# Kernel optimization log

Measured on AMD Instinct MI355X. Metric: run time of the kernel, lower is better.

The kernel has to match this reference:

```python
import jax, jax.numpy as jnp
import numpy as np

N_NODES = 100000
N_EDGES = 1600000
IN_CH = 128
HID = 128   # 2 * out_channels
OUT_CH = 64


def setup_inputs() -> dict:
    key = jax.random.key(0)
    k1, k2, k3, k4, k5, k6 = jax.random.split(key, 6)
    x = jax.random.normal(k1, (N_NODES, IN_CH), dtype=jnp.float32)
    edge_index = jax.random.randint(k2, (2, N_EDGES), 0, N_NODES, dtype=jnp.int64)
    W1 = jax.random.normal(k3, (IN_CH, HID), dtype=jnp.float32) / np.sqrt(IN_CH)
    b1 = jax.random.normal(k4, (HID,), dtype=jnp.float32) * 0.01
    W2 = jax.random.normal(k5, (HID, OUT_CH), dtype=jnp.float32) / np.sqrt(HID)
    b2 = jax.random.normal(k6, (OUT_CH,), dtype=jnp.float32) * 0.01
    return {"x": x, "edge_index": edge_index, "W1": W1, "b1": b1, "W2": W2, "b2": b2}


def _gcn_layer(x, src, dst, norm, W, b, n_nodes):
    # GCNConv: linear transform, then normalized scatter-add aggregation + bias
    h = x @ W                                   # [N, d_out]
    msg = h[src] * norm[:, None]                # gather + edge normalize, [E+N, d_out]
    out = jax.ops.segment_sum(msg, dst, num_segments=n_nodes)
    return out + b


def reference(x, edge_index, W1, b1, W2, b2):
    n = x.shape[0]
    loop = jnp.arange(n, dtype=edge_index.dtype)
    # add self-loops (PyG GCNConv default)
    src = jnp.concatenate([edge_index[0], loop])
    dst = jnp.concatenate([edge_index[1], loop])
    # symmetric normalization deg^-1/2[src] * deg^-1/2[dst]
    deg = jax.ops.segment_sum(jnp.ones_like(dst, x.dtype), dst, num_segments=n)
    dinv = jnp.where(deg > 0, jax.lax.rsqrt(deg), 0.0)
    norm = dinv[src] * dinv[dst]

    h = jax.nn.relu(_gcn_layer(x, src, dst, norm, W1, b1, n))
    out = jax.nn.relu(_gcn_layer(h, src, dst, norm, W2, b2, n))
    return out
```

## Files before the change

kernel.cpp:

```cpp
#include <hip/hip_runtime.h>
#include <hip/hip_fp16.h>

#define BSH 9
#define BSZ 512
#define CAP 12288

__global__ __launch_bounds__(256) void passA(const int* __restrict__ ei,
                                             int* __restrict__ bcount, int E, int NB) {
  __shared__ int hist[256];
  int t = threadIdx.x;
  hist[t] = 0;
  __syncthreads();
  for (int e = blockIdx.x * 256 + t; e < E; e += gridDim.x * 256)
    atomicAdd(&hist[ei[E + e] >> BSH], 1);
  __syncthreads();
  if (t < NB && hist[t]) atomicAdd(&bcount[t], hist[t]);
}

__global__ __launch_bounds__(256) void scanB(const int* __restrict__ bcount,
                                             int* __restrict__ bstart,
                                             int* __restrict__ bfill, int NB, int E) {
  __shared__ int s[256];
  int t = threadIdx.x;
  int v = (t < NB) ? bcount[t] : 0;
  s[t] = v;
  __syncthreads();
  for (int off = 1; off < 256; off <<= 1) {
    int add = (t >= off) ? s[t - off] : 0;
    __syncthreads();
    s[t] += add;
    __syncthreads();
  }
  if (t < NB) {
    int ex = s[t] - v;
    bstart[t] = ex;
    bfill[t] = ex;
  }
  if (t == 0) bstart[NB] = E;
}

template <int NT, bool IN_F16, bool SCALE>
__device__ __forceinline__ void gemm_body(const void* __restrict__ Xv,
                                          const float* __restrict__ W,
                                          const float* __restrict__ dinv,
                                          __half* __restrict__ G, int nrows, int bid,
                                          float4* Xs, float4* Ws) {
  constexpr int TN4 = NT / 64;
  constexpr int KT = 16;
  constexpr int NW4 = NT / 4;
  const float4* W4 = (const float4*)W;
  int tid = threadIdx.x;
  int tx = tid & 15, ty = (tid >> 4) & 3;
  int tyg = tid >> 4;
  int row0 = bid * 128;

  float acc[8][TN4][4];
#pragma unroll
  for (int r = 0; r < 8; ++r)
#pragma unroll
    for (int c = 0; c < TN4; ++c)
#pragma unroll
      for (int q = 0; q < 4; ++q) acc[r][c][q] = 0.f;

  for (int k0 = 0; k0 < 128; k0 += KT) {
    if constexpr (!IN_F16) {
      const float4* X4 = (const float4*)Xv;
#pragma unroll
      for (int u = 0; u < 2; ++u) {
        int f = tid + u * 256;
        int r = f >> 2, kq = f & 3;
        int gr = row0 + r;
        float4 v = {0.f, 0.f, 0.f, 0.f};
        if (gr < nrows) v = X4[gr * 32 + (k0 >> 2) + kq];
        Xs[r * 4 + kq] = v;
      }
    } else {
      const float4* X4h = (const float4*)Xv;
      int r = tid >> 1, oct = tid & 1;
      int gr = row0 + r;
      float4 raw = {0.f, 0.f, 0.f, 0.f};
      if (gr < nrows) raw = X4h[gr * 16 + (k0 >> 3) + oct];
      const __half2* hp = (const __half2*)&raw;
      float2 f0 = __half22float2(hp[0]);
      float2 f1 = __half22float2(hp[1]);
      float2 f2 = __half22float2(hp[2]);
      float2 f3 = __half22float2(hp[3]);
      Xs[r * 4 + oct * 2 + 0] = make_float4(f0.x, f0.y, f1.x, f1.y);
      Xs[r * 4 + oct * 2 + 1] = make_float4(f2.x, f2.y, f3.x, f3.y);
    }
#pragma unroll
    for (int u = 0; u < (KT * NW4 + 255) / 256; ++u) {
      int f = tid + u * 256;
      if (f < KT * NW4) {
        int k = f / NW4, c = f % NW4;
        Ws[f] = W4[(size_t)(k0 + k) * NW4 + c];
      }
    }
    __syncthreads();
#pragma unroll
    for (int k4 = 0; k4 < KT / 4; ++k4) {
      int kk4 = (k4 + ty) & 3;
      float4 xa[8];
#pragma unroll
      for (int r = 0; r < 8; ++r) xa[r] = Xs[(tyg * 8 + r) * 4 + kk4];
      float4 wv[4][TN4];
#pragma unroll
      for (int kk = 0; kk < 4; ++kk)
#pragma unroll
        for (int c = 0; c < TN4; ++c)
          wv[kk][c] = Ws[(kk4 * 4 + kk) * NW4 + tx * TN4 + c];
#pragma unroll
      for (int r = 0; r < 8; ++r) {
        float xk[4] = {xa[r].x, xa[r].y, xa[r].z, xa[r].w};
#pragma unroll
        for (int kk = 0; kk < 4; ++kk)
#pragma unroll
          for (int c = 0; c < TN4; ++c) {
            acc[r][c][0] = fmaf(xk[kk], wv[kk][c].x, acc[r][c][0]);
            acc[r][c][1] = fmaf(xk[kk], wv[kk][c].y, acc[r][c][1]);
            acc[r][c][2] = fmaf(xk[kk], wv[kk][c].z, acc[r][c][2]);
            acc[r][c][3] = fmaf(xk[kk], wv[kk][c].w, acc[r][c][3]);
          }
      }
    }
    __syncthreads();
  }
  float2* G2 = (float2*)G;
#pragma unroll
  for (int r = 0; r < 8; ++r) {
    int gr = row0 + tyg * 8 + r;
    if (gr < nrows) {
      float d = SCALE ? dinv[gr] : 1.f;
#pragma unroll
      for (int c = 0; c < TN4; ++c) {
        union { __half2 h[2]; float2 f; } u;
        u.h[0] = __floats2half2_rn(acc[r][c][0] * d, acc[r][c][1] * d);
        u.h[1] = __floats2half2_rn(acc[r][c][2] * d, acc[r][c][3] * d);
        G2[(size_t)gr * (NT / 4) + tx * TN4 + c] = u.f;
      }
    }
  }
}

__global__ __launch_bounds__(256) void fused_gemm_passB(
    const float* __restrict__ X, const float* __restrict__ W1,
    __half* __restrict__ G, int nrows, int GB,
    const int* __restrict__ ei, int* __restrict__ bfill,
    unsigned int* __restrict__ pairs, int E) {
  if ((int)blockIdx.x < GB) {
    __shared__ float4 Xs[128 * 4];
    __shared__ float4 Ws[16 * 32];
    gemm_body<128, false, false>(X, W1, nullptr, G, nrows, blockIdx.x, Xs, Ws);
  } else {
    __shared__ int hist[256];
    __shared__ int gbase[256];
    int bid = blockIdx.x - GB;
    int t = threadIdx.x;
    hist[t] = 0;
    __syncthreads();
    int d[8], s[8], lp[8], bb[8];
    int base = bid * 2048;
#pragma unroll
    for (int u = 0; u < 8; ++u) {
      int e = base + u * 256 + t;
      if (e < E) {
        d[u] = ei[E + e];
        s[u] = ei[e];
        bb[u] = d[u] >> BSH;
        lp[u] = atomicAdd(&hist[bb[u]], 1);
      } else {
        bb[u] = -1;
      }
    }
    __syncthreads();
    if (hist[t]) gbase[t] = atomicAdd(&bfill[t], hist[t]);
    __syncthreads();
#pragma unroll
    for (int u = 0; u < 8; ++u)
      if (bb[u] >= 0)
        pairs[gbase[bb[u]] + lp[u]] =
            ((unsigned int)(d[u] & (BSZ - 1)) << 17) | (unsigned int)s[u];
  }
}

__global__ __launch_bounds__(512) void passC(const unsigned int* __restrict__ pairs,
                                             const int* __restrict__ bstart,
                                             int* __restrict__ rowstart,
                                             int* __restrict__ deg,
                                             float* __restrict__ dinv,
                                             int* __restrict__ csr, int N) {
  __shared__ int hcnt[BSZ];
  __shared__ int lfill[BSZ];
  __shared__ int ss[512];
  __shared__ int lcsr[CAP];
  int b = blockIdx.x;
  int t = threadIdx.x;
  int lo = bstart[b], hi = bstart[b + 1];
  int cnt = hi - lo;
  int nbase = b << BSH;
  hcnt[t] = 0;
  __syncthreads();
  for (int k = lo + t; k < hi; k += 512)
    atomicAdd(&hcnt[(pairs[k] >> 17) & (BSZ - 1)], 1);
  __syncthreads();
  int v = hcnt[t];
  ss[t] = v;
  __syncthreads();
  for (int off = 1; off < 512; off <<= 1) {
    int add = (t >= off) ? ss[t - off] : 0;
    __syncthreads();
    ss[t] += add;
    __syncthreads();
  }
  int ex = ss[t] - v;
  lfill[t] = ex;
  int node = nbase + t;
  if (node < N) {
    rowstart[node] = lo + ex;
    deg[node] = v;
    dinv[node] = rsqrtf((float)(v + 1));
  }
  __syncthreads();
  bool fits = (cnt <= CAP);
  for (int k = lo + t; k < hi; k += 512) {
    unsigned int p = pairs[k];
    int pos = atomicAdd(&lfill[(p >> 17) & (BSZ - 1)], 1);
    int src = (int)(p & 0x1FFFFu);
    if (fits) lcsr[pos] = src;
    else      csr[lo + pos] = src;
  }
  __syncthreads();
  if (fits)
    for (int k = t; k < cnt; k += 512) csr[lo + k] = lcsr[k];
}

__global__ __launch_bounds__(256) void agg128(
    const __half* __restrict__ G, const int* __restrict__ csr,
    const int* __restrict__ rowstart, const int* __restrict__ deg,
    const float* __restrict__ dinv, const float* __restrict__ bias,
    __half* __restrict__ out, int n) {
  int wid = blockIdx.x * 4 + (threadIdx.x >> 6);
  if (wid >= n) return;
  int i = __builtin_amdgcn_readfirstlane(wid);
  int lane = threadIdx.x & 63;
  const __half2* Gp = (const __half2*)G;
  float di = dinv[i];
  float2 g = __half22float2(Gp[(size_t)i * 64 + lane]);
  float2 a = {di * g.x, di * g.y};
  int s = rowstart[i];
  int d = deg[i];
  int cnt = d < 64 ? d : 64;
  int myidx = 0;
  if (lane < cnt) myidx = csr[s + lane];
  int k = 0;
  for (; k + 3 < cnt; k += 4) {
    int s0 = __builtin_amdgcn_readfirstlane(__shfl(myidx, k));
    int s1 = __builtin_amdgcn_readfirstlane(__shfl(myidx, k + 1));
    int s2 = __builtin_amdgcn_readfirstlane(__shfl(myidx, k + 2));
    int s3 = __builtin_amdgcn_readfirstlane(__shfl(myidx, k + 3));
    float w0 = dinv[s0], w1 = dinv[s1], w2 = dinv[s2], w3 = dinv[s3];
    float2 v0 = __half22float2(Gp[(size_t)s0 * 64 + lane]);
    float2 v1 = __half22float2(Gp[(size_t)s1 * 64 + lane]);
    float2 v2 = __half22float2(Gp[(size_t)s2 * 64 + lane]);
    float2 v3 = __half22float2(Gp[(size_t)s3 * 64 + lane]);
    a.x = fmaf(w0, v0.x, a.x); a.y = fmaf(w0, v0.y, a.y);
    a.x = fmaf(w1, v1.x, a.x); a.y = fmaf(w1, v1.y, a.y);
    a.x = fmaf(w2, v2.x, a.x); a.y = fmaf(w2, v2.y, a.y);
    a.x = fmaf(w3, v3.x, a.x); a.y = fmaf(w3, v3.y, a.y);
  }
  for (; k < cnt; ++k) {
    int s0 = __builtin_amdgcn_readfirstlane(__shfl(myidx, k));
    float w0 = dinv[s0];
    float2 v0 = __half22float2(Gp[(size_t)s0 * 64 + lane]);
    a.x = fmaf(w0, v0.x, a.x); a.y = fmaf(w0, v0.y, a.y);
  }
  for (int j = s + 64; j < s + d; ++j) {
    int s0 = __builtin_amdgcn_readfirstlane(csr[j]);
    float w0 = dinv[s0];
    float2 v0 = __half22float2(Gp[(size_t)s0 * 64 + lane]);
    a.x = fmaf(w0, v0.x, a.x); a.y = fmaf(w0, v0.y, a.y);
  }
  float2 b = ((const float2*)bias)[lane];
  float ox = fmaxf(fmaf(di, a.x, b.x), 0.f);
  float oy = fmaxf(fmaf(di, a.y, b.y), 0.f);
  ((__half2*)out)[(size_t)i * 64 + lane] = __floats2half2_rn(ox, oy);
}

__global__ __launch_bounds__(256) void agg64(
    const __half* __restrict__ G, const int* __restrict__ csr,
    const int* __restrict__ rowstart, const int* __restrict__ deg,
    const float* __restrict__ dinv, const float* __restrict__ bias,
    float* __restrict__ out, int n) {
  int wid = blockIdx.x * 4 + (threadIdx.x >> 6);
  if (wid >= n) return;
  int i = __builtin_amdgcn_readfirstlane(wid);
  int lane = threadIdx.x & 63;
  float a = __half2float(G[(size_t)i * 64 + lane]);
  int s = rowstart[i];
  int d = deg[i];
  int cnt = d < 64 ? d : 64;
  int myidx = 0;
  if (lane < cnt) myidx = csr[s + lane];
  int k = 0;
  for (; k + 3 < cnt; k += 4) {
    int s0 = __builtin_amdgcn_readfirstlane(__shfl(myidx, k));
    int s1 = __builtin_amdgcn_readfirstlane(__shfl(myidx, k + 1));
    int s2 = __builtin_amdgcn_readfirstlane(__shfl(myidx, k + 2));
    int s3 = __builtin_amdgcn_readfirstlane(__shfl(myidx, k + 3));
    float v0 = __half2float(G[(size_t)s0 * 64 + lane]);
    float v1 = __half2float(G[(size_t)s1 * 64 + lane]);
    float v2 = __half2float(G[(size_t)s2 * 64 + lane]);
    float v3 = __half2float(G[(size_t)s3 * 64 + lane]);
    a += (v0 + v1) + (v2 + v3);
  }
  for (; k < cnt; ++k) {
    int s0 = __builtin_amdgcn_readfirstlane(__shfl(myidx, k));
    a += __half2float(G[(size_t)s0 * 64 + lane]);
  }
  for (int j = s + 64; j < s + d; ++j) {
    int s0 = __builtin_amdgcn_readfirstlane(csr[j]);
    a += __half2float(G[(size_t)s0 * 64 + lane]);
  }
  float o = fmaxf(fmaf(dinv[i], a, bias[lane]), 0.f);
  out[(size_t)i * 64 + lane] = o;
}

__global__ __launch_bounds__(256) void gemm64(const __half* __restrict__ X,
                                              const float* __restrict__ W,
                                              const float* __restrict__ dinv,
                                              __half* __restrict__ G, int nrows) {
  __shared__ float4 Xs[128 * 4];
  __shared__ float4 Ws[16 * 16];
  gemm_body<64, true, true>(X, W, dinv, G, nrows, blockIdx.x, Xs, Ws);
}

extern "C" void kernel_launch(void* const* d_in, const int* in_sizes, int n_in,
                              void* d_out, int out_size, void* d_ws, size_t ws_size,
                              hipStream_t stream) {
  const float* x  = (const float*)d_in[0];
  const int*   ei = (const int*)d_in[1];
  const float* W1 = (const float*)d_in[2];
  const float* b1 = (const float*)d_in[3];
  const float* W2 = (const float*)d_in[4];
  const float* b2 = (const float*)d_in[5];
  float* out = (float*)d_out;

  const int N = in_sizes[0] / 128;
  const int E = in_sizes[1] / 2;
  const int NB = (N + BSZ - 1) >> BSH;

  char* base = (char*)d_ws;
  size_t off = 0;
  auto alloc = [&](size_t bytes) -> void* {
    void* p = base + off;
    off += (bytes + 255) & ~(size_t)255;
    return p;
  };
  int*          bcount   = (int*)alloc(256 * 4);
  int*          bstart   = (int*)alloc(260 * 4);
  int*          bfill    = (int*)alloc(256 * 4);
  int*          deg      = (int*)alloc((size_t)N * 4);
  int*          rowstart = (int*)alloc((size_t)N * 4);
  float*        dinv     = (float*)alloc((size_t)N * 4);
  int*          csr      = (int*)alloc((size_t)E * 4);
  unsigned int* pairs    = (unsigned int*)alloc((size_t)E * 4);
  __half*       g1       = (__half*)alloc((size_t)N * 128 * 2);
  __half*       x2       = (__half*)alloc((size_t)N * 128 * 2);

  hipMemsetAsync(bcount, 0, 256 * 4, stream);
  passA<<<512, 256, 0, stream>>>(ei, bcount, E, NB);
  scanB<<<1, 256, 0, stream>>>(bcount, bstart, bfill, NB, E);

  int GB = (N + 127) / 128;
  int PB = (E + 2047) / 2048;
  fused_gemm_passB<<<GB + PB, 256, 0, stream>>>(x, W1, g1, N, GB, ei, bfill, pairs, E);

  passC<<<NB, 512, 0, stream>>>(pairs, bstart, rowstart, deg, dinv, csr, N);

  agg128<<<(N + 3) / 4, 256, 0, stream>>>(g1, csr, rowstart, deg, dinv, b1, x2, N);
  gemm64<<<GB, 256, 0, stream>>>(x2, W2, dinv, g1, N);
  agg64<<<(N + 3) / 4, 256, 0, stream>>>(g1, csr, rowstart, deg, dinv, b2, out, N);
}
```

Before: 325.6 us.

## Replace FP32 SIMT GEMMs with fp16 MFMA GEMMs and interleave gemm/scatter blocks

Both dense transforms are rewritten to use MFMA 16x16x32 f16 instructions. The weights are converted to fp16 and staged transposed in LDS, and A fragments are loaded straight from global memory, where the old code used blocked FP32 FMA loops. The fused kernel also interleaves GEMM blocks with edge-bucketing blocks so the compute-bound and memory-bound work overlap on the device. Inputs are rounded to fp16 before the multiply, which adds precision risk, and the output stores become scalar fp16 writes that may be less coalesced.

```diff
diff --git a/kernel.cpp b/kernel.cpp
--- a/kernel.cpp
+++ b/kernel.cpp
@@ -1,5 +1,8 @@
 #include <hip/hip_runtime.h>
 #include <hip/hip_fp16.h>
+
+typedef _Float16 f16x8 __attribute__((ext_vector_type(8)));
+typedef float f32x4 __attribute__((ext_vector_type(4)));
 
 #define BSH 9
 #define BSZ 512
@@ -39,104 +42,91 @@
   if (t == 0) bstart[NB] = E;
 }
 
-template <int NT, bool IN_F16, bool SCALE>
-__device__ __forceinline__ void gemm_body(const void* __restrict__ Xv,
-                                          const float* __restrict__ W,
-                                          const float* __restrict__ dinv,
-                                          __half* __restrict__ G, int nrows, int bid,
-                                          float4* Xs, float4* Ws) {
-  constexpr int TN4 = NT / 64;
-  constexpr int KT = 16;
-  constexpr int NW4 = NT / 4;
-  const float4* W4 = (const float4*)W;
-  int tid = threadIdx.x;
-  int tx = tid & 15, ty = (tid >> 4) & 3;
-  int tyg = tid >> 4;
-  int row0 = bid * 128;
-
-  float acc[8][TN4][4];
-#pragma unroll
-  for (int r = 0; r < 8; ++r)
-#pragma unroll
-    for (int c = 0; c < TN4; ++c)
-#pragma unroll
-      for (int q = 0; q < 4; ++q) acc[r][c][q] = 0.f;
-
-  for (int k0 = 0; k0 < 128; k0 += KT) {
-    if constexpr (!IN_F16) {
-      const float4* X4 = (const float4*)Xv;
-#pragma unroll
-      for (int u = 0; u < 2; ++u) {
-        int f = tid + u * 256;
-        int r = f >> 2, kq = f & 3;
-        int gr = row0 + r;
-        float4 v = {0.f, 0.f, 0.f, 0.f};
-        if (gr < nrows) v = X4[gr * 32 + (k0 >> 2) + kq];
-        Xs[r * 4 + kq] = v;
+template <int NC, int NWC, bool IN_F16, bool SCALE>
+__device__ __forceinline__ void gemm_mfma_body(
+    const void* __restrict__ Xv, const float* __restrict__ W,
+    const float* __restrict__ dinv, _Float16* __restrict__ G, int nrows, int bid,
+    _Float16* Bs) {
+  int t = threadIdx.x;
+  {
+    int n = t % NC;
+    int kh = (t / NC) * (NC / 2);
+    constexpr int NBLK = (NC / 2) / 8;
+#pragma unroll
+    for (int b = 0; b < NBLK; ++b) {
+      f16x8 tmp;
+#pragma unroll
+      for (int j = 0; j < 8; ++j)
+        tmp[j] = (_Float16)W[(size_t)(kh + b * 8 + j) * NC + n];
+      *(f16x8*)(&Bs[n * 136 + kh + b * 8]) = tmp;
+    }
+  }
+  __syncthreads();
+
+  int w = t >> 6, lane = t & 63;
+  int m = lane & 15, q = lane >> 4;
+  int wr = (w / NWC) * 64, wc = (w % NWC) * 64;
+  int row0 = bid * ((4 / NWC) * 64);
+
+  f32x4 acc[4][4];
+#pragma unroll
+  for (int rt = 0; rt < 4; ++rt)
+#pragma unroll
+    for (int ct = 0; ct < 4; ++ct)
+#pragma unroll
+      for (int qq = 0; qq < 4; ++qq) acc[rt][ct][qq] = 0.f;
+
+#pragma unroll
+  for (int kc = 0; kc < 4; ++kc) {
+    int kbase = kc * 32 + q * 8;
+    f16x8 af[4];
+#pragma unroll
+    for (int rt = 0; rt < 4; ++rt) {
+      int row = row0 + wr + rt * 16 + m;
+      if constexpr (IN_F16) {
+        f16x8 a = {0, 0, 0, 0, 0, 0, 0, 0};
+        if (row < nrows) a = *(const f16x8*)((const _Float16*)Xv + (size_t)row * 128 + kbase);
+        af[rt] = a;
+      } else {
+        float4 x0 = {0, 0, 0, 0}, x1 = {0, 0, 0, 0};
+        if (row < nrows) {
+          const float* Xf = (const float*)Xv;
+          x0 = *(const float4*)(Xf + (size_t)row * 128 + kbase);
+          x1 = *(const float4*)(Xf + (size_t)row * 128 + kbase + 4);
+        }
+        f16x8 a;
+        a[0] = (_Float16)x0.x; a[1] = (_Float16)x0.y;
+        a[2] = (_Float16)x0.z; a[3] = (_Float16)x0.w;
+        a[4] = (_Float16)x1.x; a[5] = (_Float16)x1.y;
+        a[6] = (_Float16)x1.z; a[7] = (_Float16)x1.w;
+        af[rt] = a;
       }
-    } else {
-      const float4* X4h = (const float4*)Xv;
-      int r = tid >> 1, oct = tid & 1;
-      int gr = row0 + r;
-      float4 raw = {0.f, 0.f, 0.f, 0.f};
-      if (gr < nrows) raw = X4h[gr * 16 + (k0 >> 3) + oct];
-      const __half2* hp = (const __half2*)&raw;
-      float2 f0 = __half22float2(hp[0]);
-      float2 f1 = __half22float2(hp[1]);
-      float2 f2 = __half22float2(hp[2]);
-      float2 f3 = __half22float2(hp[3]);
-      Xs[r * 4 + oct * 2 + 0] = make_float4(f0.x, f0.y, f1.x, f1.y);
-      Xs[r * 4 + oct * 2 + 1] = make_float4(f2.x, f2.y, f3.x, f3.y);
-    }
-#pragma unroll
-    for (int u = 0; u < (KT * NW4 + 255) / 256; ++u) {
-      int f = tid + u * 256;
-      if (f < KT * NW4) {
-        int k = f / NW4, c = f % NW4;
-        Ws[f] = W4[(size_t)(k0 + k) * NW4 + c];
-      }
-    }
-    __syncthreads();
-#pragma unroll
-    for (int k4 = 0; k4 < KT / 4; ++k4) {
-      int kk4 = (k4 + ty) & 3;
-      float4 xa[8];
-#pragma unroll
-      for (int r = 0; r < 8; ++r) xa[r] = Xs[(tyg * 8 + r) * 4 + kk4];
-      float4 wv[4][TN4];
-#pragma unroll
-      for (int kk = 0; kk < 4; ++kk)
-#pragma unroll
-        for (int c = 0; c < TN4; ++c)
-          wv[kk][c] = Ws[(kk4 * 4 + kk) * NW4 + tx * TN4 + c];
-#pragma unroll
-      for (int r = 0; r < 8; ++r) {
-        float xk[4] = {xa[r].x, xa[r].y, xa[r].z, xa[r].w};
-#pragma unroll
-        for (int kk = 0; kk < 4; ++kk)
-#pragma unroll
-          for (int c = 0; c < TN4; ++c) {
-            acc[r][c][0] = fmaf(xk[kk], wv[kk][c].x, acc[r][c][0]);
-            acc[r][c][1] = fmaf(xk[kk], wv[kk][c].y, acc[r][c][1]);
-            acc[r][c][2] = fmaf(xk[kk], wv[kk][c].z, acc[r][c][2]);
-            acc[r][c][3] = fmaf(xk[kk], wv[kk][c].w, acc[r][c][3]);
-          }
-      }
-    }
-    __syncthreads();
-  }
-  float2* G2 = (float2*)G;
-#pragma unroll
-  for (int r = 0; r < 8; ++r) {
-    int gr = row0 + tyg * 8 + r;
-    if (gr < nrows) {
-      float d = SCALE ? dinv[gr] : 1.f;
-#pragma unroll
-      for (int c = 0; c < TN4; ++c) {
-        union { __half2 h[2]; float2 f; } u;
-        u.h[0] = __floats2half2_rn(acc[r][c][0] * d, acc[r][c][1] * d);
-        u.h[1] = __floats2half2_rn(acc[r][c][2] * d, acc[r][c][3] * d);
-        G2[(size_t)gr * (NT / 4) + tx * TN4 + c] = u.f;
+    }
+    f16x8 bf[4];
+#pragma unroll
+    for (int ct = 0; ct < 4; ++ct) {
+      int n = wc + ct * 16 + m;
+      bf[ct] = *(f16x8*)(&Bs[n * 136 + kbase]);
+    }
+#pragma unroll
+    for (int rt = 0; rt < 4; ++rt)
+#pragma unroll
+      for (int ct = 0; ct < 4; ++ct)
+        acc[rt][ct] = __builtin_amdgcn_mfma_f32_16x16x32_f16(af[rt], bf[ct],
+                                                             acc[rt][ct], 0, 0, 0);
+  }
+#pragma unroll
+  for (int rt = 0; rt < 4; ++rt) {
+#pragma unroll
+    for (int r = 0; r < 4; ++r) {
+      int row = row0 + wr + rt * 16 + q * 4 + r;
+      if (row < nrows) {
+        float d = SCALE ? dinv[row] : 1.f;
+#pragma unroll
+        for (int ct = 0; ct < 4; ++ct) {
+          int col = wc + ct * 16 + m;
+          G[(size_t)row * NC + col] = (_Float16)(acc[rt][ct][r] * d);
+        }
       }
     }
   }
@@ -144,17 +134,22 @@
 
 __global__ __launch_bounds__(256) void fused_gemm_passB(
     const float* __restrict__ X, const float* __restrict__ W1,
-    __half* __restrict__ G, int nrows, int GB,
+    _Float16* __restrict__ G, int nrows, int GB,
     const int* __restrict__ ei, int* __restrict__ bfill,
-    unsigned int* __restrict__ pairs, int E) {
-  if ((int)blockIdx.x < GB) {
-    __shared__ float4 Xs[128 * 4];
-    __shared__ float4 Ws[16 * 32];
-    gemm_body<128, false, false>(X, W1, nullptr, G, nrows, blockIdx.x, Xs, Ws);
+    unsigned int* __restrict__ pairs, int E, int PB) {
+  __shared__ char smem[128 * 136 * 2];
+  int g = blockIdx.x;
+  int M2 = 2 * (GB < PB ? GB : PB);
+  bool is_gemm;
+  int bid;
+  if (g < M2) { is_gemm = (g & 1) == 0; bid = g >> 1; }
+  else        { is_gemm = (GB > PB);    bid = g - M2 + (GB < PB ? GB : PB); }
+  if (is_gemm) {
+    gemm_mfma_body<128, 2, false, false>(X, W1, nullptr, G, nrows, bid,
+                                         (_Float16*)smem);
   } else {
-    __shared__ int hist[256];
-    __shared__ int gbase[256];
-    int bid = blockIdx.x - GB;
+    int* hist = (int*)smem;
+    int* gbase = (int*)(smem + 1024);
     int t = threadIdx.x;
     hist[t] = 0;
     __syncthreads();
@@ -181,6 +176,14 @@
         pairs[gbase[bb[u]] + lp[u]] =
             ((unsigned int)(d[u] & (BSZ - 1)) << 17) | (unsigned int)s[u];
   }
+}
+
+__global__ __launch_bounds__(256) void gemm2_mfma(const _Float16* __restrict__ X,
+                                                  const float* __restrict__ W,
+                                                  const float* __restrict__ dinv,
+                                                  _Float16* __restrict__ G, int nrows) {
+  __shared__ _Float16 Bs[64 * 136];
+  gemm_mfma_body<64, 1, true, true>(X, W, dinv, G, nrows, blockIdx.x, Bs);
 }
 
 __global__ __launch_bounds__(512) void passC(const unsigned int* __restrict__ pairs,
@@ -325,15 +328,6 @@
   out[(size_t)i * 64 + lane] = o;
 }
 
-__global__ __launch_bounds__(256) void gemm64(const __half* __restrict__ X,
-                                              const float* __restrict__ W,
-                                              const float* __restrict__ dinv,
-                                              __half* __restrict__ G, int nrows) {
-  __shared__ float4 Xs[128 * 4];
-  __shared__ float4 Ws[16 * 16];
-  gemm_body<64, true, true>(X, W, dinv, G, nrows, blockIdx.x, Xs, Ws);
-}
-
 extern "C" void kernel_launch(void* const* d_in, const int* in_sizes, int n_in,
                               void* d_out, int out_size, void* d_ws, size_t ws_size,
                               hipStream_t stream) {
@@ -373,11 +367,13 @@
 
   int GB = (N + 127) / 128;
   int PB = (E + 2047) / 2048;
-  fused_gemm_passB<<<GB + PB, 256, 0, stream>>>(x, W1, g1, N, GB, ei, bfill, pairs, E);
-
+  fused_gemm_passB<<<GB + PB, 256, 0, stream>>>(x, W1, (_Float16*)g1, N, GB, ei,
+                                                bfill, pairs, E, PB);
   passC<<<NB, 512, 0, stream>>>(pairs, bstart, rowstart, deg, dinv, csr, N);
 
   agg128<<<(N + 3) / 4, 256, 0, stream>>>(g1, csr, rowstart, deg, dinv, b1, x2, N);
-  gemm64<<<GB, 256, 0, stream>>>(x2, W2, dinv, g1, N);
+  int G2B = (N + 255) / 256;
+  gemm2_mfma<<<G2B, 256, 0, stream>>>((const _Float16*)x2, W2, dinv,
+                                      (_Float16*)g1, N);
   agg64<<<(N + 3) / 4, 256, 0, stream>>>(g1, csr, rowstart, deg, dinv, b2, out, N);
 }
```

Measured after the change: 297.7 us. 1.09x faster.
